# Performance work log

Hardware: AMD Instinct MI355X
Metric: run time of the kernel (lower is better)

The kernel has to match this reference:

```python
import jax, jax.numpy as jnp
import numpy as np

H = 768
HEADS = 12
HD = H // HEADS
INTER = 3072
EPS = 1e-6


def setup_inputs() -> dict:
    key = jax.random.key(0)
    ks = jax.random.split(key, 10)
    B, T = 4, 1024
    scale = 0.02
    return {
        "x": jax.random.normal(ks[0], (B, T, H), jnp.float32),
        "mask": jnp.ones((B, T), jnp.float32),
        "w_qkv": jax.random.normal(ks[1], (H, 3 * H), jnp.float32) * scale,
        "w_o": jax.random.normal(ks[2], (H, H), jnp.float32) * scale,
        "tau": jnp.full((HEADS,), 5.0, jnp.float32),
        "w1": jax.random.normal(ks[3], (H, INTER), jnp.float32) * scale,
        "b1": jnp.zeros((INTER,), jnp.float32),
        "w2": jax.random.normal(ks[4], (INTER, H), jnp.float32) * scale,
        "b2": jnp.zeros((H,), jnp.float32),
        "nb1": jnp.zeros((H,), jnp.float32),
        "nb2": jnp.zeros((H,), jnp.float32),
    }


def _block(x, mask, w_qkv, w_o, tau, w1, b1, w2, b2, nb1, nb2):
    B, T, C = x.shape
    qkv = x @ w_qkv                                  # [B,T,3H]
    q, k, v = jnp.split(qkv, 3, axis=-1)
    q = q.reshape(B, T, HEADS, HD)
    k = k.reshape(B, T, HEADS, HD)
    v = v.reshape(B, T, HEADS, HD)
    # 2quad attention: quadratic-normalized scores instead of softmax
    s = jnp.einsum("bthd,bshd->bhts", q, k) / jnp.sqrt(jnp.float32(HD))
    s = s / tau[None, :, None, None]
    w = s * s                                        # [B,HEADS,T,T]
    w = w * mask[:, None, None, :]                   # zero masked keys
    w = w / (jnp.sum(w, axis=-1, keepdims=True) + EPS)
    out = jnp.einsum("bhts,bshd->bthd", w, v).reshape(B, T, C)
    out = out @ w_o
    x = x + 0.2 * out + nb1                          # scaled residual + bias-only norm1
    ffn = jax.nn.relu(x @ w1 + b1) @ w2 + b2
    x = x + ffn + nb2                                # residual + bias-only norm2
    return x


def reference(x, mask, w_qkv, w_o, tau, w1, b1, w2, b2, nb1, nb2):
    return _block(x, mask, w_qkv, w_o, tau, w1, b1, w2, b2, nb1, nb2)
```

## Files before the change

### kernel.cpp

```cpp
#include <hip/hip_runtime.h>

typedef __bf16 bf16x8 __attribute__((ext_vector_type(8)));
typedef float f32x4 __attribute__((ext_vector_type(4)));
typedef unsigned short u16;
typedef unsigned long long u64;

#define HDIM 768
#define NHEADS 12
#define SEQ 1024
#define NBATCH 4
#define ROWS 4096
#define QKV3 2304
#define INTERDIM 3072

__device__ __forceinline__ u16 f2bf(float f) {
  union { float f; unsigned int u; } v; v.f = f;
  unsigned int r = v.u + 0x7fffu + ((v.u >> 16) & 1u);
  return (u16)(r >> 16);
}

__device__ __forceinline__ void gload16(const u16* g, u16* l) {
  __builtin_amdgcn_global_load_lds(
      (const __attribute__((address_space(1))) void*)g,
      (__attribute__((address_space(3))) void*)l, 16, 0, 0);
}

__device__ __forceinline__ unsigned ldsoff(const void* p) {
  return (unsigned)(unsigned long long)(const __attribute__((address_space(3))) char*)p;
}

__device__ __forceinline__ u64 tr8(unsigned a) {
  u64 r;
  asm volatile("ds_read_b64_tr_b16 %0, %1" : "=v"(r) : "v"(a));
  return r;
}

union B8 { u64 q[2]; bf16x8 v; };

__global__ __launch_bounds__(256) void k_prep(
    const float* __restrict__ x, u16* __restrict__ xb,
    const float* __restrict__ wqkv, u16* __restrict__ wqkvT,
    const float* __restrict__ wo, u16* __restrict__ woT,
    const float* __restrict__ w1, u16* __restrict__ w1T,
    const float* __restrict__ w2, u16* __restrict__ w2T) {
  __shared__ float tile[32][33];
  int bid = blockIdx.x, tid = threadIdx.x;
  if (bid < 3072) {
    int i = bid * 256 + tid;
    float4 f = reinterpret_cast<const float4*>(x)[i];
    ushort4 o;
    o.x = f2bf(f.x); o.y = f2bf(f.y); o.z = f2bf(f.z); o.w = f2bf(f.w);
    reinterpret_cast<ushort4*>(xb)[i] = o;
    return;
  }
  const float* in; u16* outp; int K, N, t;
  if (bid < 4800)      { in = wqkv; outp = wqkvT; K = 768;  N = 2304; t = bid - 3072; }
  else if (bid < 5376) { in = wo;   outp = woT;   K = 768;  N = 768;  t = bid - 4800; }
  else if (bid < 7680) { in = w1;   outp = w1T;   K = 768;  N = 3072; t = bid - 5376; }
  else                 { in = w2;   outp = w2T;   K = 3072; N = 768;  t = bid - 7680; }
  int ntx = N >> 5;
  int bx = t % ntx, by = t / ntx;
  int tx = tid & 31, ty = tid >> 5;
  int n0 = bx * 32, k0 = by * 32;
#pragma unroll
  for (int i = 0; i < 32; i += 8)
    tile[ty + i][tx] = in[(size_t)(k0 + ty + i) * N + n0 + tx];
  __syncthreads();
#pragma unroll
  for (int i = 0; i < 32; i += 8)
    outp[(size_t)(n0 + ty + i) * K + k0 + tx] = f2bf(tile[tx][ty + i]);
}

template<int BN, int MODE>
__global__ __launch_bounds__(256) void k_gemm(
    const u16* __restrict__ A, const u16* __restrict__ Bt,
    int M, int N, int K, int ksplit,
    u16* __restrict__ obf, float* __restrict__ of32,
    const float* __restrict__ e1, const float* __restrict__ e2) {
  constexpr int BM = 128, BK = 32;
  constexpr int WC = (BN == 128) ? 2 : 1;
  constexpr int WR = 4 / WC;
  constexpr int WM = BM / WR;
  constexpr int WN = BN / WC;
  constexpr int MFR = WM / 16;
  constexpr int NFR = WN / 16;
  constexpr int BISS = BN / 64;
  __shared__ u16 As[2][BM * BK];
  __shared__ u16 Bs[2][BN * BK];
  int tid = threadIdx.x, lane = tid & 63, wid = tid >> 6;
  int wr = wid / WC, wc = wid % WC;
  int fr = lane & 15, fg = lane >> 4, fk = fg * 8;

  int gx = gridDim.x;
  int nwg = gx * gridDim.y;
  int orig = blockIdx.y * gx + blockIdx.x;
  int swz = (orig & 7) * (nwg >> 3) + (orig >> 3);
  int bx = swz % gx, by = swz / gx;
  int m0 = by * BM, n0 = bx * BN;
  int Kc = K / ksplit, k0 = blockIdx.z * Kc;

  f32x4 acc[MFR][NFR] = {};

  int r = tid >> 2;
  int cswz = ((tid & 3) * 8) ^ (((r >> 1) & 3) << 3);
  const u16* Ag = A + (size_t)(m0 + r) * K + k0 + cswz;
  const u16* Bg = Bt + (size_t)(n0 + r) * K + k0 + cswz;

#define STAGE(t2) do {                                                   \
    int b_ = (t2) & 1; int kt_ = (t2) * BK;                              \
    gload16(Ag + kt_, &As[b_][wid * 512]);                               \
    gload16(Ag + kt_ + (size_t)64 * K, &As[b_][2048 + wid * 512]);       \
    gload16(Bg + kt_, &Bs[b_][wid * 512]);                               \
    if constexpr (BISS == 2)                                             \
      gload16(Bg + kt_ + (size_t)64 * K, &Bs[b_][2048 + wid * 512]);     \
  } while (0)

  int ce = fk ^ (((fr >> 1) & 3) << 3);

  int nt = Kc / BK;
  STAGE(0);
  STAGE(1);

  for (int t = 0; t < nt; t++) {
    int cur = t & 1;
    if (t == nt - 1) {
      asm volatile("s_waitcnt vmcnt(0)\n\ts_barrier" ::: "memory");
    } else if constexpr (BISS == 2) {
      asm volatile("s_waitcnt vmcnt(4)\n\ts_barrier" ::: "memory");
    } else {
      asm volatile("s_waitcnt vmcnt(3)\n\ts_barrier" ::: "memory");
    }

    bf16x8 af[MFR], bv[NFR];
#pragma unroll
    for (int mi = 0; mi < MFR; mi++)
      af[mi] = *reinterpret_cast<const bf16x8*>(&As[cur][(wr * WM + mi * 16 + fr) * BK + ce]);
#pragma unroll
    for (int ni = 0; ni < NFR; ni++)
      bv[ni] = *reinterpret_cast<const bf16x8*>(&Bs[cur][(wc * WN + ni * 16 + fr) * BK + ce]);

    asm volatile("s_waitcnt lgkmcnt(0)\n\ts_barrier" ::: "memory");
    if (t + 2 < nt) STAGE(t + 2);

    __builtin_amdgcn_s_setprio(1);
#pragma unroll
    for (int mi = 0; mi < MFR; mi++)
#pragma unroll
      for (int ni = 0; ni < NFR; ni++)
        acc[mi][ni] = __builtin_amdgcn_mfma_f32_16x16x32_bf16(af[mi], bv[ni], acc[mi][ni], 0, 0, 0);
    __builtin_amdgcn_s_setprio(0);
  }
#undef STAGE

  float* part = (MODE == 3) ? of32 + (size_t)blockIdx.z * ((size_t)M * N) : of32;
#pragma unroll
  for (int mi = 0; mi < MFR; mi++) {
#pragma unroll
    for (int ni = 0; ni < NFR; ni++) {
#pragma unroll
      for (int i = 0; i < 4; i++) {
        int row = m0 + wr * WM + mi * 16 + fg * 4 + i;
        int col = n0 + wc * WN + ni * 16 + fr;
        float v = acc[mi][ni][i];
        size_t idx = (size_t)row * N + col;
        if constexpr (MODE == 0) {
          obf[idx] = f2bf(v);
        } else if constexpr (MODE == 1) {
          float t = e1[idx] + 0.2f * v + e2[col];
          of32[idx] = t;
          obf[idx] = f2bf(t);
        } else if constexpr (MODE == 2) {
          float t = v + e1[col];
          obf[idx] = f2bf(t > 0.f ? t : 0.f);
        } else {
          part[idx] = v;
        }
      }
    }
  }
}

__global__ void k_ffn2_reduce(const float* __restrict__ p, const float* __restrict__ x1f,
                              const float* __restrict__ b2, const float* __restrict__ nb2,
                              float* __restrict__ out) {
  int i = blockIdx.x * 256 + threadIdx.x;
  int col4 = (i * 4) % HDIM;
  float4 s = reinterpret_cast<const float4*>(x1f)[i];
  float4 bb = *reinterpret_cast<const float4*>(b2 + col4);
  float4 nn = *reinterpret_cast<const float4*>(nb2 + col4);
  s.x += bb.x + nn.x; s.y += bb.y + nn.y; s.z += bb.z + nn.z; s.w += bb.w + nn.w;
#pragma unroll
  for (int z = 0; z < 2; z++) {
    float4 pv = reinterpret_cast<const float4*>(p + (size_t)z * ROWS * HDIM)[i];
    s.x += pv.x; s.y += pv.y; s.z += pv.z; s.w += pv.w;
  }
  reinterpret_cast<float4*>(out)[i] = s;
}

__global__ __launch_bounds__(512) void k_attn(
    const u16* __restrict__ qkv, const float* __restrict__ mask,
    const float* __restrict__ tau, u16* __restrict__ outp) {
  __shared__ u16 Ks[64 * 72];
  __shared__ u16 Vs[64 * 64];
  __shared__ u16 Ps[8 * 1024];
  int tid = threadIdx.x, lane = tid & 63, w = tid >> 6;
  int h = blockIdx.y, b = blockIdx.z;
  int fr = lane & 15, fg = lane >> 4, fk = fg * 8;
  int rb = b * SEQ;
  float rs = 1.0f / (8.0f * tau[h]);
  float rs2 = rs * rs;

  int t0 = blockIdx.x * 128 + w * 16;
  const u16* qrow = qkv + (size_t)(rb + t0 + fr) * QKV3 + h * 64;
  bf16x8 aq0 = *reinterpret_cast<const bf16x8*>(qrow + fk);
  bf16x8 aq1 = *reinterpret_cast<const bf16x8*>(qrow + 32 + fk);

  f32x4 acco[4] = {};
  f32x4 accd = {};

  int sr = tid >> 3, c = tid & 7;
  const u16* kg = qkv + (size_t)(rb + sr) * QKV3 + HDIM + h * 64 + c * 8;
  const u16* vg = kg + HDIM;
  u16* kw = &Ks[sr * 72 + c * 8];
  u16* vw = &Vs[((sr >> 2) * 4 + (c >> 1)) * 64 + (sr & 3) * 16 + (c & 1) * 8];
  unsigned psb = ldsoff(&Ps[w * 1024]);
  unsigned vsb = ldsoff(Vs);

  __bf16 onev = (__bf16)1.0f;
  bf16x8 ones = {onev, onev, onev, onev, onev, onev, onev, onev};

  int4 kreg = *reinterpret_cast<const int4*>(kg);
  int4 vreg = *reinterpret_cast<const int4*>(vg);

  for (int st = 0; st < SEQ; st += 64) {
    __syncthreads();
    *reinterpret_cast<int4*>(kw) = kreg;
    *reinterpret_cast<int4*>(vw) = vreg;
    __syncthreads();
    if (st + 64 < SEQ) {
      kreg = *reinterpret_cast<const int4*>(kg + (size_t)(st + 64) * QKV3);
      vreg = *reinterpret_cast<const int4*>(vg + (size_t)(st + 64) * QKV3);
    }

#pragma unroll
    for (int sf = 0; sf < 4; sf++) {
      bf16x8 bk0 = *reinterpret_cast<const bf16x8*>(&Ks[(sf * 16 + fr) * 72 + fk]);
      bf16x8 bk1 = *reinterpret_cast<const bf16x8*>(&Ks[(sf * 16 + fr) * 72 + 32 + fk]);
      f32x4 s = {};
      s = __builtin_amdgcn_mfma_f32_16x16x32_bf16(aq0, bk0, s, 0, 0, 0);
      s = __builtin_amdgcn_mfma_f32_16x16x32_bf16(aq1, bk1, s, 0, 0, 0);
      float rm = rs2 * mask[b * SEQ + st + sf * 16 + fr];
      u64 pw = 0;
#pragma unroll
      for (int i = 0; i < 4; i++) {
        float wv = s[i] * s[i] * rm;
        pw |= (u64)f2bf(wv) << (16 * i);
      }
      *reinterpret_cast<u64*>(&Ps[w * 1024 + (sf * 4 + (fr >> 2)) * 64 + (fr & 3) * 16 + fg * 4]) = pw;
    }
    asm volatile("s_waitcnt lgkmcnt(0)" ::: "memory");
    __builtin_amdgcn_sched_barrier(0);

    u64 pa0 = tr8(psb + (fg * 2 + 0) * 128 + fr * 2);
    u64 pa1 = tr8(psb + (fg * 2 + 1) * 128 + fr * 2);
    u64 pa2 = tr8(psb + (8 + fg * 2 + 0) * 128 + fr * 2);
    u64 pa3 = tr8(psb + (8 + fg * 2 + 1) * 128 + fr * 2);
    u64 vb[4][4];
#pragma unroll
    for (int df = 0; df < 4; df++) {
      vb[df][0] = tr8(vsb + ((fg * 2 + 0) * 4 + df) * 128 + fr * 2);
      vb[df][1] = tr8(vsb + ((fg * 2 + 1) * 4 + df) * 128 + fr * 2);
      vb[df][2] = tr8(vsb + ((8 + fg * 2 + 0) * 4 + df) * 128 + fr * 2);
      vb[df][3] = tr8(vsb + ((8 + fg * 2 + 1) * 4 + df) * 128 + fr * 2);
    }
    asm volatile("s_waitcnt lgkmcnt(0)" ::: "memory");
    __builtin_amdgcn_sched_barrier(0);

    B8 ap0, ap1;
    ap0.q[0] = pa0; ap0.q[1] = pa1;
    ap1.q[0] = pa2; ap1.q[1] = pa3;
#pragma unroll
    for (int df = 0; df < 4; df++) {
      B8 b0, b1;
      b0.q[0] = vb[df][0]; b0.q[1] = vb[df][1];
      b1.q[0] = vb[df][2]; b1.q[1] = vb[df][3];
      acco[df] = __builtin_amdgcn_mfma_f32_16x16x32_bf16(ap0.v, b0.v, acco[df], 0, 0, 0);
      acco[df] = __builtin_amdgcn_mfma_f32_16x16x32_bf16(ap1.v, b1.v, acco[df], 0, 0, 0);
    }
    accd = __builtin_amdgcn_mfma_f32_16x16x32_bf16(ap0.v, ones, accd, 0, 0, 0);
    accd = __builtin_amdgcn_mfma_f32_16x16x32_bf16(ap1.v, ones, accd, 0, 0, 0);
  }

#pragma unroll
  for (int df = 0; df < 4; df++)
#pragma unroll
    for (int i = 0; i < 4; i++) {
      int t = t0 + fg * 4 + i;
      int col = h * 64 + df * 16 + fr;
      float o = acco[df][i] / (accd[i] + 1e-6f);
      outp[(size_t)(rb + t) * HDIM + col] = f2bf(o);
    }
}

extern "C" void kernel_launch(void* const* d_in, const int* in_sizes, int n_in,
                              void* d_out, int out_size, void* d_ws, size_t ws_size,
                              hipStream_t stream) {
  const float* x     = (const float*)d_in[0];
  const float* mask  = (const float*)d_in[1];
  const float* w_qkv = (const float*)d_in[2];
  const float* w_o   = (const float*)d_in[3];
  const float* tau   = (const float*)d_in[4];
  const float* w1    = (const float*)d_in[5];
  const float* b1    = (const float*)d_in[6];
  const float* w2    = (const float*)d_in[7];
  const float* b2    = (const float*)d_in[8];
  const float* nb1   = (const float*)d_in[9];
  const float* nb2   = (const float*)d_in[10];
  float* out = (float*)d_out;
  (void)ws_size; (void)in_sizes; (void)n_in; (void)out_size;

  char* base = (char*)d_ws;
  float* part = (float*)base;
  u16* xb    = (u16*)(base);
  u16* wqkvT = (u16*)(base + 6291456);
  u16* woT   = (u16*)(base + 9830400);
  u16* w1T   = (u16*)(base + 11010048);
  u16* qkvb  = (u16*)(base + 15728640);
  u16* attnb = (u16*)(base + 34603008);
  u16* x1b   = (u16*)(base + 40894464);
  u16* w2T   = (u16*)(base + 50331648);
  float* x1f = (float*)(base + 55050240);
  u16* hb    = (u16*)(base + 67633152);

  k_prep<<<9984, 256, 0, stream>>>(x, xb, w_qkv, wqkvT, w_o, woT, w1, w1T, w2, w2T);

  k_gemm<128, 0><<<dim3(QKV3 / 128, ROWS / 128), 256, 0, stream>>>(
      xb, wqkvT, ROWS, QKV3, HDIM, 1, qkvb, nullptr, nullptr, nullptr);
  k_attn<<<dim3(SEQ / 128, NHEADS, NBATCH), 512, 0, stream>>>(qkvb, mask, tau, attnb);
  k_gemm<64, 1><<<dim3(HDIM / 64, ROWS / 128), 256, 0, stream>>>(
      attnb, woT, ROWS, HDIM, HDIM, 1, x1b, x1f, x, nb1);
  k_gemm<128, 2><<<dim3(INTERDIM / 128, ROWS / 128), 256, 0, stream>>>(
      x1b, w1T, ROWS, INTERDIM, HDIM, 1, hb, nullptr, b1, nullptr);
  k_gemm<128, 3><<<dim3(HDIM / 128, ROWS / 128, 2), 256, 0, stream>>>(
      hb, w2T, ROWS, HDIM, INTERDIM, 2, nullptr, part, nullptr, nullptr);
  k_ffn2_reduce<<<ROWS * HDIM / 4 / 256, 256, 0, stream>>>(part, x1f, b2, nb2, out);
}
```

Measured before the change: 167.4 us.

## Use 256-row GEMM tiles, deeper split-K for FFN2, flatten attention grid

The GEMM kernel now takes BM as a template parameter. The QKV, FFN1 and FFN2 GEMMs use 256x128 tiles with a matching number of async global-to-LDS loads and vmcnt waits, and launch bounds now ask for two blocks per SM. FFN2 split-K goes from 2 to 4 partials, and the reduce kernel sums all four. The attention launch becomes a flat 1-D grid that interleaves heads and batches across consecutive blocks. The larger tiles aim to raise data reuse per block and the extra split-K aims to fill the GPU. The costs are more accumulator registers, grid sizes that may not divide evenly over the CUs (288 blocks for QKV), and more partial-sum traffic in the reduce.

```diff
diff --git a/kernel.cpp b/kernel.cpp
--- a/kernel.cpp
+++ b/kernel.cpp
@@ -71,19 +71,20 @@
     outp[(size_t)(n0 + ty + i) * K + k0 + tx] = f2bf(tile[tx][ty + i]);
 }
 
-template<int BN, int MODE>
-__global__ __launch_bounds__(256) void k_gemm(
+template<int BM, int BN, int MODE>
+__global__ __launch_bounds__(256, 2) void k_gemm(
     const u16* __restrict__ A, const u16* __restrict__ Bt,
     int M, int N, int K, int ksplit,
     u16* __restrict__ obf, float* __restrict__ of32,
     const float* __restrict__ e1, const float* __restrict__ e2) {
-  constexpr int BM = 128, BK = 32;
+  constexpr int BK = 32;
   constexpr int WC = (BN == 128) ? 2 : 1;
   constexpr int WR = 4 / WC;
   constexpr int WM = BM / WR;
   constexpr int WN = BN / WC;
   constexpr int MFR = WM / 16;
   constexpr int NFR = WN / 16;
+  constexpr int AISS = BM / 64;
   constexpr int BISS = BN / 64;
   __shared__ u16 As[2][BM * BK];
   __shared__ u16 Bs[2][BN * BK];
@@ -108,11 +109,12 @@
 
 #define STAGE(t2) do {                                                   \
     int b_ = (t2) & 1; int kt_ = (t2) * BK;                              \
-    gload16(Ag + kt_, &As[b_][wid * 512]);                               \
-    gload16(Ag + kt_ + (size_t)64 * K, &As[b_][2048 + wid * 512]);       \
-    gload16(Bg + kt_, &Bs[b_][wid * 512]);                               \
-    if constexpr (BISS == 2)                                             \
-      gload16(Bg + kt_ + (size_t)64 * K, &Bs[b_][2048 + wid * 512]);     \
+    _Pragma("unroll")                                                    \
+    for (int i_ = 0; i_ < AISS; i_++)                                    \
+      gload16(Ag + kt_ + (size_t)(i_ * 64) * K, &As[b_][i_ * 2048 + wid * 512]); \
+    _Pragma("unroll")                                                    \
+    for (int i_ = 0; i_ < BISS; i_++)                                    \
+      gload16(Bg + kt_ + (size_t)(i_ * 64) * K, &Bs[b_][i_ * 2048 + wid * 512]); \
   } while (0)
 
   int ce = fk ^ (((fr >> 1) & 3) << 3);
@@ -125,7 +127,9 @@
     int cur = t & 1;
     if (t == nt - 1) {
       asm volatile("s_waitcnt vmcnt(0)\n\ts_barrier" ::: "memory");
-    } else if constexpr (BISS == 2) {
+    } else if constexpr (AISS + BISS == 6) {
+      asm volatile("s_waitcnt vmcnt(6)\n\ts_barrier" ::: "memory");
+    } else if constexpr (AISS + BISS == 4) {
       asm volatile("s_waitcnt vmcnt(4)\n\ts_barrier" ::: "memory");
     } else {
       asm volatile("s_waitcnt vmcnt(3)\n\ts_barrier" ::: "memory");
@@ -190,7 +194,7 @@
   float4 nn = *reinterpret_cast<const float4*>(nb2 + col4);
   s.x += bb.x + nn.x; s.y += bb.y + nn.y; s.z += bb.z + nn.z; s.w += bb.w + nn.w;
 #pragma unroll
-  for (int z = 0; z < 2; z++) {
+  for (int z = 0; z < 4; z++) {
     float4 pv = reinterpret_cast<const float4*>(p + (size_t)z * ROWS * HDIM)[i];
     s.x += pv.x; s.y += pv.y; s.z += pv.z; s.w += pv.w;
   }
@@ -204,13 +208,15 @@
   __shared__ u16 Vs[64 * 64];
   __shared__ u16 Ps[8 * 1024];
   int tid = threadIdx.x, lane = tid & 63, w = tid >> 6;
-  int h = blockIdx.y, b = blockIdx.z;
+  int bid = blockIdx.x;
+  int bh = bid % 48, t0i = bid / 48;
+  int h = bh >> 2, b = bh & 3;
   int fr = lane & 15, fg = lane >> 4, fk = fg * 8;
   int rb = b * SEQ;
   float rs = 1.0f / (8.0f * tau[h]);
   float rs2 = rs * rs;
 
-  int t0 = blockIdx.x * 128 + w * 16;
+  int t0 = t0i * 128 + w * 16;
   const u16* qrow = qkv + (size_t)(rb + t0 + fr) * QKV3 + h * 64;
   bf16x8 aq0 = *reinterpret_cast<const bf16x8*>(qrow + fk);
   bf16x8 aq1 = *reinterpret_cast<const bf16x8*>(qrow + 32 + fk);
@@ -334,14 +340,14 @@
 
   k_prep<<<9984, 256, 0, stream>>>(x, xb, w_qkv, wqkvT, w_o, woT, w1, w1T, w2, w2T);
 
-  k_gemm<128, 0><<<dim3(QKV3 / 128, ROWS / 128), 256, 0, stream>>>(
+  k_gemm<256, 128, 0><<<dim3(QKV3 / 128, ROWS / 256), 256, 0, stream>>>(
       xb, wqkvT, ROWS, QKV3, HDIM, 1, qkvb, nullptr, nullptr, nullptr);
-  k_attn<<<dim3(SEQ / 128, NHEADS, NBATCH), 512, 0, stream>>>(qkvb, mask, tau, attnb);
-  k_gemm<64, 1><<<dim3(HDIM / 64, ROWS / 128), 256, 0, stream>>>(
+  k_attn<<<384, 512, 0, stream>>>(qkvb, mask, tau, attnb);
+  k_gemm<128, 64, 1><<<dim3(HDIM / 64, ROWS / 128), 256, 0, stream>>>(
       attnb, woT, ROWS, HDIM, HDIM, 1, x1b, x1f, x, nb1);
-  k_gemm<128, 2><<<dim3(INTERDIM / 128, ROWS / 128), 256, 0, stream>>>(
+  k_gemm<256, 128, 2><<<dim3(INTERDIM / 128, ROWS / 256), 256, 0, stream>>>(
       x1b, w1T, ROWS, INTERDIM, HDIM, 1, hb, nullptr, b1, nullptr);
-  k_gemm<128, 3><<<dim3(HDIM / 128, ROWS / 128, 2), 256, 0, stream>>>(
-      hb, w2T, ROWS, HDIM, INTERDIM, 2, nullptr, part, nullptr, nullptr);
+  k_gemm<256, 128, 3><<<dim3(HDIM / 128, ROWS / 256, 4), 256, 0, stream>>>(
+      hb, w2T, ROWS, HDIM, INTERDIM, 4, nullptr, part, nullptr, nullptr);
   k_ffn2_reduce<<<ROWS * HDIM / 4 / 256, 256, 0, stream>>>(part, x1f, b2, nb2, out);
 }
```

Result: faster. 155.1 us (-7.3%).
